# Kernel tuning notes

Measured on AMD Instinct MI355X. Metric: run time of the kernel, lower is better.

## Reference

```python
import jax, jax.numpy as jnp
import numpy as np
from jax import lax

DIM = 512
HEADS = 8
HEAD_DIM = 64  # max(16, dim // num_heads)
INNER = HEADS * HEAD_DIM
REGION_SIZE = 32
EPEG_K = 5
SCALE = HEAD_DIM ** -0.5


def setup_inputs() -> dict:
    key = jax.random.key(0)
    ks = jax.random.split(key, 7)
    B, L = 1, 16384
    x = jax.random.normal(ks[0], (B, L, DIM), jnp.float32)
    qkv_w = jax.random.normal(ks[1], (3 * INNER, DIM), jnp.float32) * 0.02
    qkv_b = jax.random.normal(ks[2], (3 * INNER,), jnp.float32) * 0.02
    proj_w = jax.random.normal(ks[3], (DIM, INNER), jnp.float32) * 0.02
    proj_b = jax.random.normal(ks[4], (DIM,), jnp.float32) * 0.02
    epeg_w = jax.random.normal(ks[5], (HEADS, 1, EPEG_K, 1), jnp.float32) * 0.02
    epeg_b = jax.random.normal(ks[6], (HEADS,), jnp.float32) * 0.02
    return {"x": x, "qkv_w": qkv_w, "qkv_b": qkv_b, "proj_w": proj_w,
            "proj_b": proj_b, "epeg_w": epeg_w, "epeg_b": epeg_b}


def _forward(x, qkv_w, qkv_b, proj_w, proj_b, epeg_w, epeg_b):
    B, L, C = x.shape
    # _grid_pad: fold tokens onto square grid, pad to multiple of region_size
    Hs = int(np.ceil(np.sqrt(L)))
    Hs += (-Hs) % REGION_SIZE
    Ws = Hs
    r = REGION_SIZE
    add_len = Hs * Ws - L
    if add_len > 0:
        x = jnp.pad(x, ((0, 0), (0, add_len), (0, 0)))
    # region_partition: [B,H,W,C] -> [B*nW, r*r, C]
    xg = x.reshape(B, Hs // r, r, Ws // r, r, C)
    xg = xg.transpose(0, 1, 3, 2, 4, 5).reshape(-1, r * r, C)
    N = r * r
    # InnerAttention
    qkv = (xg @ qkv_w.T + qkv_b).reshape(-1, N, 3, HEADS, HEAD_DIM)
    qkv = qkv.transpose(2, 0, 3, 1, 4)  # [3, Bw, h, N, d]
    q, k, v = qkv[0], qkv[1], qkv[2]
    attn = jnp.einsum('bhid,bhjd->bhij', q * SCALE, k)  # [Bw, h, N, N]
    # EPEG: depthwise (k,1) conv over the attention-logit map
    pad = EPEG_K // 2
    conv = lax.conv_general_dilated(
        attn, epeg_w, window_strides=(1, 1),
        padding=((pad, pad), (0, 0)),
        dimension_numbers=('NCHW', 'OIHW', 'NCHW'),
        feature_group_count=HEADS) + epeg_b.reshape(1, HEADS, 1, 1)
    attn = jax.nn.softmax(attn + conv, axis=-1)
    out = jnp.einsum('bhij,bhjd->bhid', attn, v)  # [Bw, h, N, d]
    out = out.transpose(0, 2, 1, 3).reshape(-1, N, INNER)
    out = out @ proj_w.T + proj_b
    # region_reverse: [B*nW, r, r, C] -> [B, H*W, C]
    out = out.reshape(B, Hs // r, Ws // r, r, r, C)
    out = out.transpose(0, 1, 3, 2, 4, 5).reshape(B, Hs * Ws, C)
    if add_len > 0:
        out = out[:, :L]
    return out


def reference(x, qkv_w, qkv_b, proj_w, proj_b, epeg_w, epeg_b):
    return _forward(x, qkv_w, qkv_b, proj_w, proj_b, epeg_w, epeg_b)
```

## Files before the change

kernel.cpp:

```cpp
#include <hip/hip_runtime.h>


using bf16x8 = __attribute__((ext_vector_type(8))) short;
using f32x4  = __attribute__((ext_vector_type(4))) float;

__device__ __forceinline__ unsigned short f2bf(float f) {
    unsigned u = __float_as_uint(f);
    u += 0x7fff + ((u >> 16) & 1);
    return (unsigned short)(u >> 16);
}
__device__ __forceinline__ float bf2f(unsigned short s) {
    return __uint_as_float(((unsigned)s) << 16);
}
__device__ __forceinline__ unsigned cvtpk(float lo, float hi) {
    unsigned r;
    asm("v_cvt_pk_bf16_f32 %0, %1, %2" : "=v"(r) : "v"(lo), "v"(hi));
    return r;
}
__device__ __forceinline__ void gload16(const void* g, void* l) {
    __builtin_amdgcn_global_load_lds(
        (const __attribute__((address_space(1))) void*)g,
        (__attribute__((address_space(3))) void*)l, 16, 0, 0);
}
__device__ __forceinline__ int l_from_rn(int region, int n) {
    int gi = region >> 2, gj = region & 3;
    int a = n >> 5, b = n & 31;
    return ((gi * 32 + a) << 7) + (gj << 5) + b;
}

__global__ __launch_bounds__(256) void cast_x_kernel(
    const float* __restrict__ x, unsigned short* __restrict__ xb)
{
    int tid = threadIdx.x;
    int t = blockIdx.x * 4 + (tid >> 6);
    int c8 = tid & 63;
    int l = l_from_rn(t >> 10, t & 1023);
    const float* src = x + (size_t)l * 512 + c8 * 8;
    float4 a = *(const float4*)src;
    float4 b = *(const float4*)(src + 4);
    bf16x8 o;
    o[0] = (short)f2bf(a.x); o[1] = (short)f2bf(a.y);
    o[2] = (short)f2bf(a.z); o[3] = (short)f2bf(a.w);
    o[4] = (short)f2bf(b.x); o[5] = (short)f2bf(b.y);
    o[6] = (short)f2bf(b.z); o[7] = (short)f2bf(b.w);
    *(bf16x8*)(xb + (size_t)t * 512 + c8 * 8) = o;
}

__global__ __launch_bounds__(256) void cast_w_kernel(
    const float* __restrict__ w, unsigned short* __restrict__ wb)
{
    int g = blockIdx.x * 256 + threadIdx.x;
    const float* src = w + (size_t)g * 8;
    float4 a = *(const float4*)src;
    float4 b = *(const float4*)(src + 4);
    bf16x8 o;
    o[0] = (short)f2bf(a.x); o[1] = (short)f2bf(a.y);
    o[2] = (short)f2bf(a.z); o[3] = (short)f2bf(a.w);
    o[4] = (short)f2bf(b.x); o[5] = (short)f2bf(b.y);
    o[6] = (short)f2bf(b.z); o[7] = (short)f2bf(b.w);
    *(bf16x8*)(wb + (size_t)g * 8) = o;
}

__global__ __launch_bounds__(256) void qkv_kernel(
    const unsigned short* __restrict__ xb, const unsigned short* __restrict__ wb,
    const float* __restrict__ bias, unsigned short* __restrict__ qo,
    unsigned short* __restrict__ ko, unsigned short* __restrict__ vto)
{
    __shared__ __align__(16) unsigned short As[128 * 64];
    __shared__ __align__(16) unsigned short Bs[128 * 64];
    const int c0t = blockIdx.x * 128;
    const int t0 = blockIdx.y * 128;
    const int tid = threadIdx.x;
    const int lane = tid & 63, w = tid >> 6;
    const int arow = lane & 15, kgrp = lane >> 4;
    const int wr = w >> 1, wc = w & 1;

    f32x4 acc[4][4];
    #pragma unroll
    for (int m = 0; m < 4; ++m)
        #pragma unroll
        for (int n = 0; n < 4; ++n) {
            f32x4 z = {0.f, 0.f, 0.f, 0.f};
            acc[m][n] = z;
        }

    for (int k0 = 0; k0 < 512; k0 += 64) {
        __syncthreads();
        #pragma unroll
        for (int it = 0; it < 4; ++it) {
            int slot = it * 256 + tid;
            int row = slot >> 3, phys = slot & 7;
            int c8 = phys ^ (row & 7);
            gload16(xb + (size_t)(t0 + row) * 512 + k0 + c8 * 8,
                    &As[(it * 256 + (w << 6)) * 8]);
            gload16(wb + (size_t)(c0t + row) * 512 + k0 + c8 * 8,
                    &Bs[(it * 256 + (w << 6)) * 8]);
        }
        __syncthreads();

        bf16x8 af[4][2], bfr[4][2];
        #pragma unroll
        for (int m = 0; m < 4; ++m) {
            int r = wr * 64 + m * 16 + arow;
            af[m][0] = *(const bf16x8*)&As[r * 64 + ((kgrp ^ (r & 7)) * 8)];
            af[m][1] = *(const bf16x8*)&As[r * 64 + (((4 + kgrp) ^ (r & 7)) * 8)];
        }
        #pragma unroll
        for (int n = 0; n < 4; ++n) {
            int r = wc * 64 + n * 16 + arow;
            bfr[n][0] = *(const bf16x8*)&Bs[r * 64 + ((kgrp ^ (r & 7)) * 8)];
            bfr[n][1] = *(const bf16x8*)&Bs[r * 64 + (((4 + kgrp) ^ (r & 7)) * 8)];
        }
        #pragma unroll
        for (int m = 0; m < 4; ++m)
            #pragma unroll
            for (int n = 0; n < 4; ++n) {
                acc[m][n] = __builtin_amdgcn_mfma_f32_16x16x32_bf16(
                    af[m][0], bfr[n][0], acc[m][n], 0, 0, 0);
                acc[m][n] = __builtin_amdgcn_mfma_f32_16x16x32_bf16(
                    af[m][1], bfr[n][1], acc[m][n], 0, 0, 0);
            }
    }

    const int s = c0t >> 9;
    const int region = t0 >> 10;
    const float qs = (s == 0) ? 0.18033688f : 1.0f;
    #pragma unroll
    for (int n = 0; n < 4; ++n) {
        int cg = c0t + wc * 64 + n * 16 + arow;
        float bi = bias[cg];
        int h = (cg >> 6) & 7, d = cg & 63;
        if (s < 2) {
            unsigned short* dst = (s == 0) ? qo : ko;
            #pragma unroll
            for (int m = 0; m < 4; ++m) {
                int tb = t0 + wr * 64 + m * 16 + kgrp * 4;
                unsigned short* p =
                    dst + ((size_t)(region * 8 + h) * 1024 + (tb & 1023)) * 64 + d;
                #pragma unroll
                for (int i = 0; i < 4; ++i)
                    p[(size_t)i * 64] = f2bf((acc[m][n][i] + bi) * qs);
            }
        } else {
            #pragma unroll
            for (int m = 0; m < 4; ++m) {
                int tb = t0 + wr * 64 + m * 16 + kgrp * 4;
                ushort4 pk;
                pk.x = f2bf(acc[m][n][0] + bi);
                pk.y = f2bf(acc[m][n][1] + bi);
                pk.z = f2bf(acc[m][n][2] + bi);
                pk.w = f2bf(acc[m][n][3] + bi);
                *(ushort4*)(vto + (size_t)(region * 8 + h) * 65536 +
                            (size_t)d * 1024 + (tb & 1023)) = pk;
            }
        }
    }
}

__global__ __launch_bounds__(256) void attn_kernel(
    const unsigned short* __restrict__ qg, const unsigned short* __restrict__ kg,
    const unsigned short* __restrict__ vtg, const float* __restrict__ epw,
    const float* __restrict__ epb, unsigned short* __restrict__ ao)
{
    const int bid = blockIdx.x;
    const int wid = (bid & 7) * 128 + (bid >> 3);
    const int rb = wid & 7;
    const int rh = wid >> 3;
    const int head = rh & 7, region = rh >> 3;
    const unsigned short* qb = qg + (size_t)rh * 65536;
    const unsigned short* kb = kg + (size_t)rh * 65536;
    const unsigned short* vb = vtg + (size_t)rh * 65536;
    const int i0 = rb * 128;
    const int tid = threadIdx.x;
    const int lane = tid & 63, w = tid >> 6;
    const int arow = lane & 15, kgrp = lane >> 4;

    __shared__ __align__(16) unsigned short Ks[2][4096];
    __shared__ __align__(16) unsigned short VTs[2][4096];
    __shared__ float row_l[128];

    float c_[5];
    #pragma unroll
    for (int t = 0; t < 5; ++t) c_[t] = epw[head * 5 + t];
    c_[2] += 1.0f;

    bf16x8 qtf[2][2];
    #pragma unroll
    for (int m = 0; m < 2; ++m) {
        int gr = i0 + w * 32 + m * 16 + arow;
        float av[8], bv[8];
        #pragma unroll
        for (int e = 0; e < 8; ++e) { av[e] = 0.f; bv[e] = 0.f; }
        #pragma unroll
        for (int t = 0; t < 5; ++t) {
            int r = gr + t - 2;
            if (r >= 0 && r < 1024) {
                const unsigned short* p = qb + (size_t)r * 64 + kgrp * 8;
                bf16x8 a = *(const bf16x8*)p;
                bf16x8 b = *(const bf16x8*)(p + 32);
                float ct = c_[t];
                #pragma unroll
                for (int e = 0; e < 8; ++e) {
                    av[e] += ct * bf2f((unsigned short)a[e]);
                    bv[e] += ct * bf2f((unsigned short)b[e]);
                }
            }
        }
        union { unsigned u[4]; bf16x8 v; } pa, pb;
        #pragma unroll
        for (int e2 = 0; e2 < 4; ++e2) {
            pa.u[e2] = cvtpk(av[e2 * 2], av[e2 * 2 + 1]);
            pb.u[e2] = cvtpk(bv[e2 * 2], bv[e2 * 2 + 1]);
        }
        qtf[m][0] = pa.v;
        qtf[m][1] = pb.v;
    }

    f32x4 oacc[2][4];
    #pragma unroll
    for (int m = 0; m < 2; ++m)
        #pragma unroll
        for (int dt = 0; dt < 4; ++dt) {
            f32x4 z = {0.f, 0.f, 0.f, 0.f};
            oacc[m][dt] = z;
        }
    float lp[2] = {0.f, 0.f};

    auto stage = [&](int jt, int buf) {
        const int j0 = jt * 64;
        #pragma unroll
        for (int it = 0; it < 2; ++it) {
            int q_ = (it * 4 + w) * 64 + lane;
            int row = q_ >> 3, phys = q_ & 7, c8 = phys ^ (row & 7);
            gload16(kb + (size_t)(j0 + row) * 64 + c8 * 8,
                    &Ks[buf][(it * 4 + w) * 512]);
            gload16(vb + (size_t)row * 1024 + j0 + c8 * 8,
                    &VTs[buf][(it * 4 + w) * 512]);
        }
    };

    stage(0, 0);

    for (int jt = 0; jt < 16; ++jt) {
        const int cur = jt & 1;
        __syncthreads();
        if (jt < 15) stage(jt + 1, cur ^ 1);

        const unsigned short* Kc = &Ks[cur][0];
        const unsigned short* Vc = &VTs[cur][0];
        char* const pbase = (w < 2) ? (char*)&Ks[cur][0] : (char*)&VTs[cur][0];
        const int plrow0 = (w & 1) * 32 + arow;

        bf16x8 vf[4][2];
        #pragma unroll
        for (int dt = 0; dt < 4; ++dt) {
            int drow = dt * 16 + arow;
            vf[dt][0] = *(const bf16x8*)&Vc[drow * 64 + ((kgrp ^ (drow & 7)) * 8)];
            vf[dt][1] = *(const bf16x8*)&Vc[drow * 64 + (((4 + kgrp) ^ (drow & 7)) * 8)];
        }

        uint2 pu[4][2];
        __builtin_amdgcn_s_setprio(1);
        #pragma unroll
        for (int ct = 0; ct < 4; ++ct) {
            int krow = ct * 16 + arow;
            bf16x8 kf0 = *(const bf16x8*)&Kc[krow * 64 + ((kgrp ^ (krow & 7)) * 8)];
            bf16x8 kf1 = *(const bf16x8*)&Kc[krow * 64 + (((4 + kgrp) ^ (krow & 7)) * 8)];
            #pragma unroll
            for (int m = 0; m < 2; ++m) {
                f32x4 sacc = {0.f, 0.f, 0.f, 0.f};
                sacc = __builtin_amdgcn_mfma_f32_16x16x32_bf16(kf0, qtf[m][0], sacc, 0, 0, 0);
                sacc = __builtin_amdgcn_mfma_f32_16x16x32_bf16(kf1, qtf[m][1], sacc, 0, 0, 0);
                float p0 = exp2f(sacc[0]), p1 = exp2f(sacc[1]);
                float p2 = exp2f(sacc[2]), p3 = exp2f(sacc[3]);
                lp[m] += (p0 + p1) + (p2 + p3);
                pu[ct][m].x = cvtpk(p0, p1);
                pu[ct][m].y = cvtpk(p2, p3);
            }
        }
        __builtin_amdgcn_s_setprio(0);
        asm volatile("s_waitcnt lgkmcnt(0)\n\ts_barrier" ::: "memory");

        #pragma unroll
        for (int ct = 0; ct < 4; ++ct)
            #pragma unroll
            for (int m = 0; m < 2; ++m)
                *(uint2*)(pbase + (plrow0 + m * 16) * 128 +
                          (((2 * ct + (kgrp >> 1)) ^ (arow & 7)) << 4) +
                          ((kgrp & 1) << 3)) = pu[ct][m];
        __builtin_amdgcn_sched_barrier(0);
        __builtin_amdgcn_s_setprio(1);
        #pragma unroll
        for (int m = 0; m < 2; ++m) {
            const char* prow = pbase + (plrow0 + m * 16) * 128;
            bf16x8 pf0 = *(const bf16x8*)(prow + ((kgrp ^ (arow & 7)) << 4));
            bf16x8 pf1 = *(const bf16x8*)(prow + (((4 + kgrp) ^ (arow & 7)) << 4));
            #pragma unroll
            for (int dt = 0; dt < 4; ++dt) {
                oacc[m][dt] = __builtin_amdgcn_mfma_f32_16x16x32_bf16(
                    pf0, vf[dt][0], oacc[m][dt], 0, 0, 0);
                oacc[m][dt] = __builtin_amdgcn_mfma_f32_16x16x32_bf16(
                    pf1, vf[dt][1], oacc[m][dt], 0, 0, 0);
            }
        }
        __builtin_amdgcn_s_setprio(0);
    }

    #pragma unroll
    for (int m = 0; m < 2; ++m) {
        float s = lp[m];
        s += __shfl_xor(s, 16);
        s += __shfl_xor(s, 32);
        if (kgrp == 0) row_l[w * 32 + m * 16 + arow] = s;
    }
    __syncthreads();
    #pragma unroll
    for (int m = 0; m < 2; ++m) {
        float inv[4];
        #pragma unroll
        for (int i = 0; i < 4; ++i)
            inv[i] = 1.f / row_l[w * 32 + m * 16 + kgrp * 4 + i];
        #pragma unroll
        for (int dt = 0; dt < 4; ++dt) {
            #pragma unroll
            for (int i = 0; i < 4; ++i) {
                size_t t = (size_t)region * 1024 + i0 + w * 32 + m * 16 + kgrp * 4 + i;
                ao[t * 512 + head * 64 + dt * 16 + arow] = f2bf(oacc[m][dt][i] * inv[i]);
            }
        }
    }
}

__global__ __launch_bounds__(256) void proj_kernel(
    const unsigned short* __restrict__ ab, const unsigned short* __restrict__ wb,
    const float* __restrict__ bias, float* __restrict__ out)
{
    __shared__ __align__(16) unsigned short As[128 * 64];
    __shared__ __align__(16) unsigned short Bs[128 * 64];
    const int c0t = blockIdx.x * 128;
    const int t0 = blockIdx.y * 128;
    const int tid = threadIdx.x;
    const int lane = tid & 63, w = tid >> 6;
    const int arow = lane & 15, kgrp = lane >> 4;
    const int wr = w >> 1, wc = w & 1;

    f32x4 acc[4][4];
    #pragma unroll
    for (int m = 0; m < 4; ++m)
        #pragma unroll
        for (int n = 0; n < 4; ++n) {
            f32x4 z = {0.f, 0.f, 0.f, 0.f};
            acc[m][n] = z;
        }

    for (int k0 = 0; k0 < 512; k0 += 64) {
        __syncthreads();
        #pragma unroll
        for (int it = 0; it < 4; ++it) {
            int slot = it * 256 + tid;
            int row = slot >> 3, phys = slot & 7;
            int c8 = phys ^ (row & 7);
            gload16(ab + (size_t)(t0 + row) * 512 + k0 + c8 * 8,
                    &As[(it * 256 + (w << 6)) * 8]);
            gload16(wb + (size_t)(c0t + row) * 512 + k0 + c8 * 8,
                    &Bs[(it * 256 + (w << 6)) * 8]);
        }
        __syncthreads();

        bf16x8 af[4][2], bfr[4][2];
        #pragma unroll
        for (int m = 0; m < 4; ++m) {
            int r = wr * 64 + m * 16 + arow;
            af[m][0] = *(const bf16x8*)&As[r * 64 + ((kgrp ^ (r & 7)) * 8)];
            af[m][1] = *(const bf16x8*)&As[r * 64 + (((4 + kgrp) ^ (r & 7)) * 8)];
        }
        #pragma unroll
        for (int n = 0; n < 4; ++n) {
            int r = wc * 64 + n * 16 + arow;
            bfr[n][0] = *(const bf16x8*)&Bs[r * 64 + ((kgrp ^ (r & 7)) * 8)];
            bfr[n][1] = *(const bf16x8*)&Bs[r * 64 + (((4 + kgrp) ^ (r & 7)) * 8)];
        }
        #pragma unroll
        for (int m = 0; m < 4; ++m)
            #pragma unroll
            for (int n = 0; n < 4; ++n) {
                acc[m][n] = __builtin_amdgcn_mfma_f32_16x16x32_bf16(
                    af[m][0], bfr[n][0], acc[m][n], 0, 0, 0);
                acc[m][n] = __builtin_amdgcn_mfma_f32_16x16x32_bf16(
                    af[m][1], bfr[n][1], acc[m][n], 0, 0, 0);
            }
    }

    #pragma unroll
    for (int n = 0; n < 4; ++n) {
        int cg = c0t + wc * 64 + n * 16 + arow;
        float bi = bias[cg];
        #pragma unroll
        for (int m = 0; m < 4; ++m) {
            int tb = t0 + wr * 64 + m * 16 + kgrp * 4;
            int l0 = l_from_rn(tb >> 10, tb & 1023);
            float* p = out + (size_t)l0 * 512 + cg;
            #pragma unroll
            for (int i = 0; i < 4; ++i)
                p[(size_t)i * 512] = acc[m][n][i] + bi;
        }
    }
}

extern "C" void kernel_launch(void* const* d_in, const int* in_sizes, int n_in,
                              void* d_out, int out_size, void* d_ws, size_t ws_size,
                              hipStream_t stream) {
    const float* x      = (const float*)d_in[0];
    const float* qkv_w  = (const float*)d_in[1];
    const float* qkv_b  = (const float*)d_in[2];
    const float* proj_w = (const float*)d_in[3];
    const float* proj_b = (const float*)d_in[4];
    const float* epeg_w = (const float*)d_in[5];
    const float* epeg_b = (const float*)d_in[6];
    float* out = (float*)d_out;

    const size_t NTOK = (size_t)16384 * 512;
    unsigned short* xb    = (unsigned short*)d_ws;
    unsigned short* wqkv  = xb + NTOK;
    unsigned short* wproj = wqkv + (size_t)1536 * 512;
    unsigned short* qb    = wproj + (size_t)512 * 512;
    unsigned short* kb    = qb + NTOK;
    unsigned short* vtb   = kb + NTOK;
    unsigned short* ao    = vtb + NTOK;

    cast_x_kernel<<<4096, 256, 0, stream>>>(x, xb);
    cast_w_kernel<<<384, 256, 0, stream>>>(qkv_w, wqkv);
    cast_w_kernel<<<128, 256, 0, stream>>>(proj_w, wproj);
    {
        dim3 grid(12, 128);
        qkv_kernel<<<grid, 256, 0, stream>>>(xb, wqkv, qkv_b, qb, kb, vtb);
    }
    attn_kernel<<<1024, 256, 0, stream>>>(qb, kb, vtb, epeg_w, epeg_b, ao);
    {
        dim3 grid(4, 128);
        proj_kernel<<<grid, 256, 0, stream>>>(ao, wproj, proj_b, out);
    }
}
```

Measured before the change: 147.0 us.

## Keep P in registers for PV MFMA and merge cast kernels

The attention kernel no longer writes the softmax probabilities to LDS and reads them back after a barrier. Instead it swaps the MFMA operand roles so the per-lane P fragments computed by the QK^T MFMA feed the PV MFMA directly. V fragments are loaded to match that layout. Output normalization now uses the row sum held in registers and writes packed bf16, which removes the shared row_l array and a __syncthreads. The three cast kernels are also merged into one launch, removing launch overhead in exchange for a branch per block.

```diff
diff --git a/kernel.cpp b/kernel.cpp
--- a/kernel.cpp
+++ b/kernel.cpp
@@ -28,14 +28,30 @@
     return ((gi * 32 + a) << 7) + (gj << 5) + b;
 }
 
-__global__ __launch_bounds__(256) void cast_x_kernel(
-    const float* __restrict__ x, unsigned short* __restrict__ xb)
+__global__ __launch_bounds__(256) void cast_all_kernel(
+    const float* __restrict__ x, const float* __restrict__ qkv_w,
+    const float* __restrict__ proj_w, unsigned short* __restrict__ xb,
+    unsigned short* __restrict__ wqkv, unsigned short* __restrict__ wproj)
 {
-    int tid = threadIdx.x;
-    int t = blockIdx.x * 4 + (tid >> 6);
-    int c8 = tid & 63;
-    int l = l_from_rn(t >> 10, t & 1023);
-    const float* src = x + (size_t)l * 512 + c8 * 8;
+    const int bid = blockIdx.x;
+    const int tid = threadIdx.x;
+    const float* src;
+    unsigned short* dst;
+    if (bid < 4096) {
+        int t = bid * 4 + (tid >> 6);
+        int c8 = tid & 63;
+        int l = l_from_rn(t >> 10, t & 1023);
+        src = x + (size_t)l * 512 + c8 * 8;
+        dst = xb + (size_t)t * 512 + c8 * 8;
+    } else if (bid < 4480) {
+        size_t g = (size_t)(bid - 4096) * 256 + tid;
+        src = qkv_w + g * 8;
+        dst = wqkv + g * 8;
+    } else {
+        size_t g = (size_t)(bid - 4480) * 256 + tid;
+        src = proj_w + g * 8;
+        dst = wproj + g * 8;
+    }
     float4 a = *(const float4*)src;
     float4 b = *(const float4*)(src + 4);
     bf16x8 o;
@@ -43,22 +59,7 @@
     o[2] = (short)f2bf(a.z); o[3] = (short)f2bf(a.w);
     o[4] = (short)f2bf(b.x); o[5] = (short)f2bf(b.y);
     o[6] = (short)f2bf(b.z); o[7] = (short)f2bf(b.w);
-    *(bf16x8*)(xb + (size_t)t * 512 + c8 * 8) = o;
-}
-
-__global__ __launch_bounds__(256) void cast_w_kernel(
-    const float* __restrict__ w, unsigned short* __restrict__ wb)
-{
-    int g = blockIdx.x * 256 + threadIdx.x;
-    const float* src = w + (size_t)g * 8;
-    float4 a = *(const float4*)src;
-    float4 b = *(const float4*)(src + 4);
-    bf16x8 o;
-    o[0] = (short)f2bf(a.x); o[1] = (short)f2bf(a.y);
-    o[2] = (short)f2bf(a.z); o[3] = (short)f2bf(a.w);
-    o[4] = (short)f2bf(b.x); o[5] = (short)f2bf(b.y);
-    o[6] = (short)f2bf(b.z); o[7] = (short)f2bf(b.w);
-    *(bf16x8*)(wb + (size_t)g * 8) = o;
+    *(bf16x8*)dst = o;
 }
 
 __global__ __launch_bounds__(256) void qkv_kernel(
@@ -177,7 +178,6 @@
 
     __shared__ __align__(16) unsigned short Ks[2][4096];
     __shared__ __align__(16) unsigned short VTs[2][4096];
-    __shared__ float row_l[128];
 
     float c_[5];
     #pragma unroll
@@ -248,15 +248,20 @@
 
         const unsigned short* Kc = &Ks[cur][0];
         const unsigned short* Vc = &VTs[cur][0];
-        char* const pbase = (w < 2) ? (char*)&Ks[cur][0] : (char*)&VTs[cur][0];
-        const int plrow0 = (w & 1) * 32 + arow;
-
-        bf16x8 vf[4][2];
+
+        bf16x8 vfa[4][2];
         #pragma unroll
         for (int dt = 0; dt < 4; ++dt) {
-            int drow = dt * 16 + arow;
-            vf[dt][0] = *(const bf16x8*)&Vc[drow * 64 + ((kgrp ^ (drow & 7)) * 8)];
-            vf[dt][1] = *(const bf16x8*)&Vc[drow * 64 + (((4 + kgrp) ^ (drow & 7)) * 8)];
+            const char* vrow = (const char*)Vc + (dt * 16 + arow) * 128;
+            #pragma unroll
+            for (int cp = 0; cp < 2; ++cp) {
+                union { uint2 u2[2]; bf16x8 v; } a;
+                int s0 = (cp * 4 + (kgrp >> 1)) ^ (arow & 7);
+                int s1 = (cp * 4 + 2 + (kgrp >> 1)) ^ (arow & 7);
+                a.u2[0] = *(const uint2*)(vrow + (s0 << 4) + ((kgrp & 1) << 3));
+                a.u2[1] = *(const uint2*)(vrow + (s1 << 4) + ((kgrp & 1) << 3));
+                vfa[dt][cp] = a.v;
+            }
         }
 
         uint2 pu[4][2];
@@ -278,29 +283,17 @@
                 pu[ct][m].y = cvtpk(p2, p3);
             }
         }
-        __builtin_amdgcn_s_setprio(0);
-        asm volatile("s_waitcnt lgkmcnt(0)\n\ts_barrier" ::: "memory");
-
-        #pragma unroll
-        for (int ct = 0; ct < 4; ++ct)
-            #pragma unroll
-            for (int m = 0; m < 2; ++m)
-                *(uint2*)(pbase + (plrow0 + m * 16) * 128 +
-                          (((2 * ct + (kgrp >> 1)) ^ (arow & 7)) << 4) +
-                          ((kgrp & 1) << 3)) = pu[ct][m];
-        __builtin_amdgcn_sched_barrier(0);
-        __builtin_amdgcn_s_setprio(1);
         #pragma unroll
         for (int m = 0; m < 2; ++m) {
-            const char* prow = pbase + (plrow0 + m * 16) * 128;
-            bf16x8 pf0 = *(const bf16x8*)(prow + ((kgrp ^ (arow & 7)) << 4));
-            bf16x8 pf1 = *(const bf16x8*)(prow + (((4 + kgrp) ^ (arow & 7)) << 4));
-            #pragma unroll
-            for (int dt = 0; dt < 4; ++dt) {
-                oacc[m][dt] = __builtin_amdgcn_mfma_f32_16x16x32_bf16(
-                    pf0, vf[dt][0], oacc[m][dt], 0, 0, 0);
-                oacc[m][dt] = __builtin_amdgcn_mfma_f32_16x16x32_bf16(
-                    pf1, vf[dt][1], oacc[m][dt], 0, 0, 0);
+            #pragma unroll
+            for (int cp = 0; cp < 2; ++cp) {
+                union { uint2 u2[2]; bf16x8 v; } pb;
+                pb.u2[0] = pu[2 * cp][m];
+                pb.u2[1] = pu[2 * cp + 1][m];
+                #pragma unroll
+                for (int dt = 0; dt < 4; ++dt)
+                    oacc[m][dt] = __builtin_amdgcn_mfma_f32_16x16x32_bf16(
+                        vfa[dt][cp], pb.v, oacc[m][dt], 0, 0, 0);
             }
         }
         __builtin_amdgcn_s_setprio(0);
@@ -311,22 +304,15 @@
         float s = lp[m];
         s += __shfl_xor(s, 16);
         s += __shfl_xor(s, 32);
-        if (kgrp == 0) row_l[w * 32 + m * 16 + arow] = s;
-    }
-    __syncthreads();
-    #pragma unroll
-    for (int m = 0; m < 2; ++m) {
-        float inv[4];
-        #pragma unroll
-        for (int i = 0; i < 4; ++i)
-            inv[i] = 1.f / row_l[w * 32 + m * 16 + kgrp * 4 + i];
+        float inv = 1.f / s;
+        size_t t = (size_t)region * 1024 + i0 + w * 32 + m * 16 + arow;
+        unsigned short* base = ao + t * 512 + head * 64;
         #pragma unroll
         for (int dt = 0; dt < 4; ++dt) {
-            #pragma unroll
-            for (int i = 0; i < 4; ++i) {
-                size_t t = (size_t)region * 1024 + i0 + w * 32 + m * 16 + kgrp * 4 + i;
-                ao[t * 512 + head * 64 + dt * 16 + arow] = f2bf(oacc[m][dt][i] * inv[i]);
-            }
+            uint2 o;
+            o.x = cvtpk(oacc[m][dt][0] * inv, oacc[m][dt][1] * inv);
+            o.y = cvtpk(oacc[m][dt][2] * inv, oacc[m][dt][3] * inv);
+            *(uint2*)(base + dt * 16 + kgrp * 4) = o;
         }
     }
 }
@@ -428,9 +414,7 @@
     unsigned short* vtb   = kb + NTOK;
     unsigned short* ao    = vtb + NTOK;
 
-    cast_x_kernel<<<4096, 256, 0, stream>>>(x, xb);
-    cast_w_kernel<<<384, 256, 0, stream>>>(qkv_w, wqkv);
-    cast_w_kernel<<<128, 256, 0, stream>>>(proj_w, wproj);
+    cast_all_kernel<<<4608, 256, 0, stream>>>(x, qkv_w, proj_w, xb, wqkv, wproj);
     {
         dim3 grid(12, 128);
         qkv_kernel<<<grid, 256, 0, stream>>>(xb, wqkv, qkv_b, qb, kb, vtb);
```

Result: no change. 148.6 us (+1.1%).
